# Kernel optimization log

Measured on AMD Instinct MI355X. Metric: run time of the kernel, lower is better.

## Reference

```python
import jax, jax.numpy as jnp
import numpy as np
from jax import lax

H, P, N, G, K, CHUNK = 64, 64, 128, 1, 4, 256
D_MODEL = 2048
D_INNER = H * P            # 4096
CONV_DIM = D_INNER + 2 * G * N  # 4352
EPS = 1e-5


def setup_inputs() -> dict:
    key = jax.random.key(0)
    ks = jax.random.split(key, 6)
    s = lambda k, shape, scale: jax.random.normal(k, shape, jnp.float32) * scale
    return {
        "hidden_states": s(ks[0], (2, 2048, D_MODEL), 1.0),
        "in_proj_w": s(ks[1], (D_MODEL, D_INNER + CONV_DIM + H), D_MODEL ** -0.5),
        "conv_w": s(ks[2], (CONV_DIM, K), K ** -0.5),
        "conv_b": jnp.zeros((CONV_DIM,), jnp.float32),
        "dt_bias": jnp.ones((H,), jnp.float32),
        "A_log": jnp.log(jnp.arange(1, H + 1, dtype=jnp.float32)),
        "D_param": jnp.ones((H,), jnp.float32),
        "norm_w": jnp.ones((D_INNER,), jnp.float32),
        "out_proj_w": s(ks[3], (D_INNER, D_MODEL), D_INNER ** -0.5),
    }


def _mamba2_forward(hidden_states, in_proj_w, conv_w, conv_b, dt_bias, A_log, D_param, norm_w, out_proj_w):
    b, l, _ = hidden_states.shape
    c = l // CHUNK  # number of chunks

    # in_proj -> gate | conv channels (x,B,C) | dt
    proj = hidden_states @ in_proj_w
    gate = proj[..., :D_INNER]
    hbc = proj[..., D_INNER:D_INNER + CONV_DIM]
    dt = proj[..., D_INNER + CONV_DIM:]  # [b,l,H]

    # depthwise causal conv1d + silu
    xt = hbc.transpose(0, 2, 1)  # [b, CONV_DIM, l]
    y = lax.conv_general_dilated(
        xt, conv_w[:, None, :], window_strides=(1,), padding=[(K - 1, 0)],
        feature_group_count=CONV_DIM, dimension_numbers=("NCH", "OIH", "NCH"))
    hbc = jax.nn.silu(y + conv_b[None, :, None]).transpose(0, 2, 1)  # [b,l,CONV_DIM]

    # split into x / B / C per group (unflatten over groups as in torch code)
    per_g = D_INNER // G
    hg = hbc.reshape(b, l, G, per_g + 2 * N)
    x = hg[..., :per_g].reshape(b, l, H, P)                 # [b,l,h,p]
    Bm = hg[..., per_g:per_g + N]                            # [b,l,g,n]
    Cm = hg[..., per_g + N:]                                 # [b,l,g,n]
    hpg = H // G
    Bh = jnp.repeat(Bm, hpg, axis=2)                         # [b,l,h,n]
    Ch = jnp.repeat(Cm, hpg, axis=2)

    # dt: softplus(dt + bias), clamp per time_step_limit (0, inf)
    dt = jax.nn.softplus(dt + dt_bias)                       # [b,l,h]
    A = -jnp.exp(A_log)                                      # [h]

    # chunk the sequence
    x_c = x.reshape(b, c, CHUNK, H, P)
    B_c = Bh.reshape(b, c, CHUNK, H, N)
    C_c = Ch.reshape(b, c, CHUNK, H, N)
    dt_c = dt.reshape(b, c, CHUNK, H)

    dA = dt_c * A[None, None, None, :]                       # [b,c,L,h]
    cum = jnp.cumsum(dA, axis=2)                             # [b,c,L,h]

    # intra-chunk (diagonal block): decay[i,j] = exp(cum_i - cum_j), i>=j
    diff = cum[:, :, :, None, :] - cum[:, :, None, :, :]     # [b,c,i,j,h]
    i = jnp.arange(CHUNK)
    mask = i[:, None] >= i[None, :]
    decay = jnp.exp(jnp.where(mask[None, None, :, :, None], diff, -jnp.inf))
    scores = jnp.einsum("bcihn,bcjhn->bcijh", C_c, B_c) * decay * dt_c[:, :, None, :, :]
    Y_diag = jnp.einsum("bcijh,bcjhp->bcihp", scores, x_c)   # [b,c,L,h,p]

    # per-chunk final states
    decay_states = jnp.exp(cum[:, :, -1:, :] - cum)          # [b,c,L,h]
    states = jnp.einsum("bclh,bclhn,bclhp->bchpn", decay_states * dt_c, B_c, x_c)
    chunk_decay = jnp.exp(cum[:, :, -1, :])                  # [b,c,h]

    # inter-chunk recurrence over chunks
    def step(prev, inp):
        st, cd = inp  # [b,h,p,n], [b,h]
        new = cd[:, :, None, None] * prev + st
        return new, prev

    init = jnp.zeros((b, H, P, N), hidden_states.dtype)
    _, prev_states = lax.scan(step, init, (jnp.moveaxis(states, 1, 0), jnp.moveaxis(chunk_decay, 1, 0)))
    prev_states = jnp.moveaxis(prev_states, 0, 1)            # [b,c,h,p,n]

    state_decay_out = jnp.exp(cum)                           # [b,c,L,h]
    Y_off = jnp.einsum("bclhn,bchpn,bclh->bclhp", C_c, prev_states, state_decay_out)

    yh = (Y_diag + Y_off).reshape(b, l, H, P) + D_param[None, None, :, None] * x
    yr = yh.reshape(b, l, D_INNER)

    # gated RMSNorm
    hidden = yr * jax.nn.silu(gate)
    var = jnp.mean(hidden * hidden, axis=-1, keepdims=True)
    hidden = hidden * lax.rsqrt(var + EPS) * norm_w

    return hidden @ out_proj_w


def reference(hidden_states, in_proj_w, conv_w, conv_b, dt_bias, A_log, D_param, norm_w, out_proj_w):
    return _mamba2_forward(hidden_states, in_proj_w, conv_w, conv_b, dt_bias, A_log, D_param, norm_w, out_proj_w)
```

## Files before the change

### kernel.cpp

```cpp
#include <hip/hip_runtime.h>
#include <hip/hip_bf16.h>


typedef __attribute__((ext_vector_type(8))) _Float16 f16x8;
typedef __attribute__((ext_vector_type(4))) float f32x4;

#define GLD16(gp, lp) __builtin_amdgcn_global_load_lds( \
    (__attribute__((address_space(1))) void*)(gp),      \
    (__attribute__((address_space(3))) void*)(lp), 16, 0, 0)

__device__ __forceinline__ unsigned short f2h(float v) {
  _Float16 h = (_Float16)v;
  return *reinterpret_cast<unsigned short*>(&h);
}
__device__ __forceinline__ float h2f(unsigned short u) {
  _Float16 h = *reinterpret_cast<_Float16*>(&u);
  return (float)h;
}
__device__ __forceinline__ float siluf(float x) { return x / (1.f + expf(-x)); }

__global__ __launch_bounds__(256) void cast_f16(const float* __restrict__ s,
                                                _Float16* __restrict__ d) {
  long i = ((long)blockIdx.x * 256 + threadIdx.x) * 4;
  float4 v = *reinterpret_cast<const float4*>(s + i);
  ushort4 u;
  u.x = f2h(v.x); u.y = f2h(v.y); u.z = f2h(v.z); u.w = f2h(v.w);
  *reinterpret_cast<ushort4*>(d + i) = u;
}

__global__ __launch_bounds__(256) void transpose_win(const float* __restrict__ src,
                                                     _Float16* __restrict__ dst) {
  __shared__ float tile[32][33];
  int c0 = blockIdx.x * 32, r0 = blockIdx.y * 32;
  int tx = threadIdx.x, ty = threadIdx.y;
#pragma unroll
  for (int i = 0; i < 4; i++)
    tile[ty + i * 8][tx] = src[(long)(r0 + ty + i * 8) * 8512 + c0 + tx];
  __syncthreads();
#pragma unroll
  for (int i = 0; i < 4; i++) {
    int c = c0 + ty + i * 8, r = r0 + tx;
    dst[(long)c * 2048 + r] = (_Float16)tile[tx][ty + i * 8];
  }
}

__global__ __launch_bounds__(256) void transpose_wout(const float* __restrict__ src,
                                                      _Float16* __restrict__ dst,
                                                      int R, int C) {
  __shared__ float tile[32][33];
  int c0 = blockIdx.x * 32, r0 = blockIdx.y * 32;
  int tx = threadIdx.x, ty = threadIdx.y;
#pragma unroll
  for (int i = 0; i < 4; i++)
    tile[ty + i * 8][tx] = src[(long)(r0 + ty + i * 8) * C + c0 + tx];
  __syncthreads();
#pragma unroll
  for (int i = 0; i < 4; i++) {
    int c = c0 + ty + i * 8, r = r0 + tx;
    dst[(long)c * R + r] = (_Float16)tile[tx][ty + i * 8];
  }
}

__global__ __launch_bounds__(512, 2) void gemm_in8(const _Float16* __restrict__ A,
                                                   const _Float16* __restrict__ Bt,
                                                   _Float16* __restrict__ gate,
                                                   float* __restrict__ hbcf) {
  __shared__ char ldsB[131072];
  const int tid = threadIdx.x;
  const int lane = tid & 63;
  const int wv = tid >> 6;
  const int wr = wv >> 2, wc = wv & 3;
  const int wg = blockIdx.x;
  const int swz = (wg & 7) * 66 + (wg >> 3);
  const int bx = swz % 33, by = swz / 33;

  const int srow = tid >> 3;
  const int scolg = (tid & 7) ^ ((srow & 4) >> 1);
  const _Float16* Ab = A + (long)by * 256 * 2048 + (long)srow * 2048 + scolg * 8;
  const _Float16* Bb = Bt + (long)bx * 256 * 2048 + (long)srow * 2048 + scolg * 8;
  const int ldst = tid << 4;

#define STAGE_A(tau, h) do {                                              \
    const _Float16* g_ = Ab + (long)(h) * 262144 + (tau) * 64;            \
    char* l_ = ldsB + ((((tau) & 1) << 2) + (h)) * 16384 + ldst;          \
    GLD16(g_, l_); GLD16(g_ + 131072, l_ + 8192); } while (0)
#define STAGE_B(tau, h) do {                                              \
    const _Float16* g_ = Bb + (long)(h) * 262144 + (tau) * 64;            \
    char* l_ = ldsB + ((((tau) & 1) << 2) + 2 + (h)) * 16384 + ldst;      \
    GLD16(g_, l_); GLD16(g_ + 131072, l_ + 8192); } while (0)

  const int fr = lane & 15;
  const int fkA = (lane >> 4) ^ ((fr & 4) ? 2 : 0);
  const char* aRd = ldsB + wr * 16384 + fr * 128 + fkA * 16;
  const char* bRd = ldsB + (2 + (wc >> 1)) * 16384 + ((wc & 1) * 64 + fr) * 128 + fkA * 16;
#define RD_A(b, mi, k32) (*(const f16x8*)(aRd + (b) * 65536 + (mi) * 2048 + (k32) * 64))
#define RD_B(b, ni, k32) (*(const f16x8*)(bRd + (b) * 65536 + (ni) * 2048 + (k32) * 64))

#define BAR() __builtin_amdgcn_s_barrier()
#define WLG0() asm volatile("s_waitcnt lgkmcnt(0)" ::: "memory")
#define WLG8() asm volatile("s_waitcnt lgkmcnt(8)" ::: "memory")
#define WVM4() asm volatile("s_waitcnt vmcnt(4)" ::: "memory")

  f32x4 acc[8][4];
#pragma unroll
  for (int mi = 0; mi < 8; ++mi)
#pragma unroll
    for (int ni = 0; ni < 4; ++ni) acc[mi][ni] = f32x4{0.f, 0.f, 0.f, 0.f};

  STAGE_A(0, 0); STAGE_A(0, 1); STAGE_B(0, 0); STAGE_B(0, 1);
  STAGE_B(1, 0); STAGE_B(1, 1);
  WVM4(); BAR();

#define MFMA_Q(MI0, MI1, x0, x1, x2, x3, PB)                                        \
  __builtin_amdgcn_s_setprio(1);                                                    \
  _Pragma("unroll") for (int ni = 0; ni < 4; ++ni) {                                \
    acc[MI0][ni] = __builtin_amdgcn_mfma_f32_16x16x32_f16(x0, PB[ni][0], acc[MI0][ni], 0, 0, 0); \
    acc[MI0][ni] = __builtin_amdgcn_mfma_f32_16x16x32_f16(x1, PB[ni][1], acc[MI0][ni], 0, 0, 0); \
    acc[MI1][ni] = __builtin_amdgcn_mfma_f32_16x16x32_f16(x2, PB[ni][0], acc[MI1][ni], 0, 0, 0); \
    acc[MI1][ni] = __builtin_amdgcn_mfma_f32_16x16x32_f16(x3, PB[ni][1], acc[MI1][ni], 0, 0, 0); \
  }                                                                                 \
  __builtin_amdgcn_s_setprio(0);

  for (int u = 0; u < 16; ++u) {
    const int t1 = 2 * u + 1;
    const int t2 = (2 * u + 2) & 31;
    const int t3 = (2 * u + 3) & 31;
    f16x8 PB0[4][2];
#pragma unroll
    for (int ni = 0; ni < 4; ++ni) { PB0[ni][0] = RD_B(0, ni, 0); PB0[ni][1] = RD_B(0, ni, 1); }
    {
      f16x8 x0 = RD_A(0, 0, 0), x1 = RD_A(0, 0, 1), x2 = RD_A(0, 1, 0), x3 = RD_A(0, 1, 1);
      STAGE_A(t1, 0); WLG8(); BAR(); WLG0();
      MFMA_Q(0, 1, x0, x1, x2, x3, PB0) BAR();
    }
    {
      f16x8 x0 = RD_A(0, 2, 0), x1 = RD_A(0, 2, 1), x2 = RD_A(0, 3, 0), x3 = RD_A(0, 3, 1);
      STAGE_A(t1, 1); BAR(); WLG0();
      MFMA_Q(2, 3, x0, x1, x2, x3, PB0) BAR();
    }
    {
      f16x8 x0 = RD_A(0, 4, 0), x1 = RD_A(0, 4, 1), x2 = RD_A(0, 5, 0), x3 = RD_A(0, 5, 1);
      STAGE_B(t2, 0); BAR(); WLG0();
      MFMA_Q(4, 5, x0, x1, x2, x3, PB0) BAR();
    }
    {
      f16x8 x0 = RD_A(0, 6, 0), x1 = RD_A(0, 6, 1), x2 = RD_A(0, 7, 0), x3 = RD_A(0, 7, 1);
      STAGE_B(t2, 1); BAR(); WLG0();
      MFMA_Q(6, 7, x0, x1, x2, x3, PB0) WVM4(); BAR();
    }
    f16x8 PB1[4][2];
#pragma unroll
    for (int ni = 0; ni < 4; ++ni) { PB1[ni][0] = RD_B(1, ni, 0); PB1[ni][1] = RD_B(1, ni, 1); }
    {
      f16x8 x0 = RD_A(1, 0, 0), x1 = RD_A(1, 0, 1), x2 = RD_A(1, 1, 0), x3 = RD_A(1, 1, 1);
      STAGE_A(t2, 0); WLG8(); BAR(); WLG0();
      MFMA_Q(0, 1, x0, x1, x2, x3, PB1) BAR();
    }
    {
      f16x8 x0 = RD_A(1, 2, 0), x1 = RD_A(1, 2, 1), x2 = RD_A(1, 3, 0), x3 = RD_A(1, 3, 1);
      STAGE_A(t2, 1); BAR(); WLG0();
      MFMA_Q(2, 3, x0, x1, x2, x3, PB1) BAR();
    }
    {
      f16x8 x0 = RD_A(1, 4, 0), x1 = RD_A(1, 4, 1), x2 = RD_A(1, 5, 0), x3 = RD_A(1, 5, 1);
      STAGE_B(t3, 0); BAR(); WLG0();
      MFMA_Q(4, 5, x0, x1, x2, x3, PB1) BAR();
    }
    {
      f16x8 x0 = RD_A(1, 6, 0), x1 = RD_A(1, 6, 1), x2 = RD_A(1, 7, 0), x3 = RD_A(1, 7, 1);
      STAGE_B(t3, 1); BAR(); WLG0();
      MFMA_Q(6, 7, x0, x1, x2, x3, PB1) WVM4(); BAR();
    }
  }
  const int m0 = by * 256 + wr * 128;
  const int n0 = bx * 256 + wc * 64;
  const int cl = lane & 15, rq = (lane >> 4) * 4;
  if (bx < 16) {
#pragma unroll
    for (int mi = 0; mi < 8; ++mi)
#pragma unroll
      for (int r = 0; r < 4; ++r) {
        long rowoff = (long)(m0 + mi * 16 + rq + r) * 4096 + n0 + cl;
#pragma unroll
        for (int ni = 0; ni < 4; ++ni) gate[rowoff + ni * 16] = (_Float16)acc[mi][ni][r];
      }
  } else {
#pragma unroll
    for (int mi = 0; mi < 8; ++mi)
#pragma unroll
      for (int r = 0; r < 4; ++r) {
        long rowoff = (long)(m0 + mi * 16 + rq + r) * 4352 + (n0 - 4096) + cl;
#pragma unroll
        for (int ni = 0; ni < 4; ++ni) hbcf[rowoff + ni * 16] = acc[mi][ni][r];
      }
  }
#undef STAGE_A
#undef STAGE_B
#undef RD_A
#undef RD_B
#undef BAR
#undef WLG0
#undef WLG8
#undef WVM4
#undef MFMA_Q
}

__global__ __launch_bounds__(256) void gemm_bt(const _Float16* __restrict__ A,
                                               const _Float16* __restrict__ Bt,
                                               float* __restrict__ Cf,
                                               int K, int ldc,
                                               long zsA, long zsB, long zsC) {
  __shared__ uint4 As4[512];
  __shared__ uint4 Bs4[512];
  _Float16* As = (_Float16*)As4;
  _Float16* Bs = (_Float16*)Bs4;
  const int tid = threadIdx.x;
  const int wv = tid >> 6;
  const int lane = tid & 63;
  const _Float16* Ab = A + (long)blockIdx.z * zsA + (long)blockIdx.y * 128 * K;
  const _Float16* Bb = Bt + (long)blockIdx.z * zsB + (long)blockIdx.x * 128 * K;
  const int c0 = wv * 128 + lane;
  const int c1 = c0 + 64;
  const long ra0 = (long)(c0 >> 2) * K + (c0 & 3) * 8;
  const long ra1 = (long)(c1 >> 2) * K + (c1 & 3) * 8;
  f32x4 acc[4][4];
#pragma unroll
  for (int mi = 0; mi < 4; mi++)
#pragma unroll
    for (int ni = 0; ni < 4; ni++) acc[mi][ni] = f32x4{0.f, 0.f, 0.f, 0.f};
  const int mrow = (wv & 1) * 64 + (lane & 15);
  const int nrow = (wv >> 1) * 64 + (lane & 15);
  const int koff = (lane >> 4) * 8;
  for (int k0 = 0; k0 < K; k0 += 32) {
    GLD16(Ab + ra0 + k0, (char*)As + c0 * 16);
    GLD16(Ab + ra1 + k0, (char*)As + c1 * 16);
    GLD16(Bb + ra0 + k0, (char*)Bs + c0 * 16);
    GLD16(Bb + ra1 + k0, (char*)Bs + c1 * 16);
    __syncthreads();
    f16x8 af[4], bfr[4];
#pragma unroll
    for (int mi = 0; mi < 4; mi++)
      af[mi] = *(const f16x8*)(As + (mrow + mi * 16) * 32 + koff);
#pragma unroll
    for (int ni = 0; ni < 4; ni++)
      bfr[ni] = *(const f16x8*)(Bs + (nrow + ni * 16) * 32 + koff);
#pragma unroll
    for (int mi = 0; mi < 4; mi++)
#pragma unroll
      for (int ni = 0; ni < 4; ni++)
        acc[mi][ni] = __builtin_amdgcn_mfma_f32_16x16x32_f16(af[mi], bfr[ni],
                                                             acc[mi][ni], 0, 0, 0);
    __syncthreads();
  }
  const int m0 = blockIdx.y * 128 + (wv & 1) * 64;
  const int n0 = blockIdx.x * 128 + (wv >> 1) * 64;
  const int cl = lane & 15, rq = (lane >> 4) * 4;
  const long zc = (long)blockIdx.z * zsC;
#pragma unroll
  for (int mi = 0; mi < 4; mi++)
#pragma unroll
    for (int r = 0; r < 4; r++) {
      long rowoff = zc + (long)(m0 + mi * 16 + rq + r) * ldc + n0 + cl;
#pragma unroll
      for (int ni = 0; ni < 4; ni++) Cf[rowoff + ni * 16] = acc[mi][ni][r];
    }
}

__global__ __launch_bounds__(256) void dtz_kernel(const float* __restrict__ hs,
                                                  const float* __restrict__ Win,
                                                  float* __restrict__ zf) {
  __shared__ float Xs[4][2048];
  int t0 = blockIdx.x * 4;
  int tid = threadIdx.x;
#pragma unroll
  for (int i = 0; i < 8; i++) {
    int e = tid * 4 + i * 1024;
    int tok = e >> 11, k = e & 2047;
    *reinterpret_cast<float4*>(&Xs[tok][k]) =
        *reinterpret_cast<const float4*>(&hs[(long)(t0 + tok) * 2048 + k]);
  }
  __syncthreads();
  int h = tid & 63, tg = tid >> 6;
  float a0 = 0.f, a1 = 0.f, a2 = 0.f, a3 = 0.f;
  const float* wcol = Win + 8448 + h;
  for (int k = 0; k < 2048; k += 4) {
    a0 = fmaf(Xs[tg][k + 0], wcol[(long)(k + 0) * 8512], a0);
    a1 = fmaf(Xs[tg][k + 1], wcol[(long)(k + 1) * 8512], a1);
    a2 = fmaf(Xs[tg][k + 2], wcol[(long)(k + 2) * 8512], a2);
    a3 = fmaf(Xs[tg][k + 3], wcol[(long)(k + 3) * 8512], a3);
  }
  zf[(long)(t0 + tg) * 64 + h] = (a0 + a1) + (a2 + a3);
}

__global__ __launch_bounds__(256) void conv_silu_kernel(const float* __restrict__ hbcf,
                                                        const float* __restrict__ convw,
                                                        const float* __restrict__ convb,
                                                        _Float16* __restrict__ x16,
                                                        _Float16* __restrict__ B16,
                                                        _Float16* __restrict__ C16) {
  int q = blockIdx.x * 256 + threadIdx.x;
  int t = blockIdx.y;
  int l = t & 2047;
  const float* col = hbcf + (long)t * 4352 + q;
  float4 wq = *reinterpret_cast<const float4*>(convw + q * 4);
  float a = convb[q];
  if (l >= 3) a += col[-3 * 4352] * wq.x;
  if (l >= 2) a += col[-2 * 4352] * wq.y;
  if (l >= 1) a += col[-1 * 4352] * wq.z;
  a += col[0] * wq.w;
  _Float16 o = (_Float16)siluf(a);
  if (q < 4096) x16[(long)t * 4096 + q] = o;
  else if (q < 4224) B16[(long)t * 128 + (q - 4096)] = o;
  else C16[(long)t * 128 + (q - 4224)] = o;
}

__global__ __launch_bounds__(256) void xtrans(const unsigned short* __restrict__ src,
                                              unsigned short* __restrict__ dst) {
  __shared__ unsigned short tile[64][66];
  int c0 = blockIdx.x * 64, r0 = blockIdx.y * 64;
  int tx = threadIdx.x & 15, ty = threadIdx.x >> 4;
#pragma unroll
  for (int i = 0; i < 4; i++) {
    int r = ty + i * 16;
    ushort4 v = *(const ushort4*)&src[(long)(r0 + r) * 4096 + c0 + 4 * tx];
    tile[r][4 * tx] = v.x; tile[r][4 * tx + 1] = v.y;
    tile[r][4 * tx + 2] = v.z; tile[r][4 * tx + 3] = v.w;
  }
  __syncthreads();
#pragma unroll
  for (int i = 0; i < 4; i++) {
    int c = ty + i * 16;
    ushort4 v;
    v.x = tile[4 * tx + 0][c]; v.y = tile[4 * tx + 1][c];
    v.z = tile[4 * tx + 2][c]; v.w = tile[4 * tx + 3][c];
    *(ushort4*)&dst[(long)(c0 + c) * 4096 + r0 + 4 * tx] = v;
  }
}

__global__ __launch_bounds__(256) void dt_cum_kernel(const float* __restrict__ zf,
                                                     const float* __restrict__ dtb,
                                                     const float* __restrict__ Alog,
                                                     float* __restrict__ dt_f,
                                                     float* __restrict__ cum_f,
                                                     float* __restrict__ cuml) {
  int bc = blockIdx.x;
  int h = threadIdx.x & 63, seg = threadIdx.x >> 6;
  int t0 = bc * 256;
  float Ah = -expf(Alog[h]);
  float bias = dtb[h];
  __shared__ float segsum[4][64];
  float s = 0.f;
  for (int j = 0; j < 64; j++) {
    int t = t0 + seg * 64 + j;
    float z = zf[(long)t * 64 + h] + bias;
    float v = (z > 20.f) ? z : log1pf(expf(z));
    dt_f[(long)t * 64 + h] = v;
    s += v * Ah;
  }
  segsum[seg][h] = s;
  __syncthreads();
  float run = 0.f;
  for (int k = 0; k < seg; k++) run += segsum[k][h];
  for (int j = 0; j < 64; j++) {
    int t = t0 + seg * 64 + j;
    run += dt_f[(long)t * 64 + h] * Ah;
    cum_f[(long)t * 64 + h] = run;
  }
  if (seg == 3) cuml[bc * 64 + h] = run;
}

__global__ __launch_bounds__(256) void states_mfma(const unsigned short* __restrict__ xT16,
                                                   const unsigned short* __restrict__ B16,
                                                   const float* __restrict__ dt_f,
                                                   const float* __restrict__ cum_f,
                                                   const float* __restrict__ cuml,
                                                   float* __restrict__ states) {
  int h = blockIdx.x, bc = blockIdx.y;
  int t0 = bc * 256, tid = threadIdx.x;
  __shared__ float w_s[256];
  __shared__ unsigned short Aw[64 * 40];
  __shared__ unsigned short BT[128 * 40];
  {
    int t = t0 + tid;
    w_s[tid] = expf(cuml[bc * 64 + h] - cum_f[(long)t * 64 + h]) * dt_f[(long)t * 64 + h];
  }
  __syncthreads();
  int wv = tid >> 6, lane = tid & 63;
  int mr = lane & 15, koff = (lane >> 4) * 8;
  f32x4 acc[4][2];
#pragma unroll
  for (int mi = 0; mi < 4; mi++)
#pragma unroll
    for (int nj = 0; nj < 2; nj++) acc[mi][nj] = f32x4{0.f, 0.f, 0.f, 0.f};
  for (int kt = 0; kt < 8; kt++) {
    {
      int p = tid >> 2, tq = tid & 3;
      const unsigned short* g = &xT16[((long)(h * 64 + p)) * 4096 + t0 + kt * 32 + tq * 8];
      ushort4 u0 = *(const ushort4*)g, u1 = *(const ushort4*)(g + 4);
      const float* wp = &w_s[kt * 32 + tq * 8];
      ushort4 o0, o1;
      o0.x = f2h(h2f(u0.x) * wp[0]); o0.y = f2h(h2f(u0.y) * wp[1]);
      o0.z = f2h(h2f(u0.z) * wp[2]); o0.w = f2h(h2f(u0.w) * wp[3]);
      o1.x = f2h(h2f(u1.x) * wp[4]); o1.y = f2h(h2f(u1.y) * wp[5]);
      o1.z = f2h(h2f(u1.z) * wp[6]); o1.w = f2h(h2f(u1.w) * wp[7]);
      *(ushort4*)&Aw[p * 40 + tq * 8] = o0;
      *(ushort4*)&Aw[p * 40 + tq * 8 + 4] = o1;
    }
    {
      int tl = tid >> 3, ng = tid & 7;
      const unsigned short* g = &B16[((long)(t0 + kt * 32 + tl)) * 128 + ng * 16];
#pragma unroll
      for (int j = 0; j < 16; j++) BT[(ng * 16 + j) * 40 + tl] = g[j];
    }
    __syncthreads();
    f16x8 af[4], bf[2];
#pragma unroll
    for (int mi = 0; mi < 4; mi++)
      af[mi] = *(const f16x8*)&Aw[(mi * 16 + mr) * 40 + koff];
#pragma unroll
    for (int nj = 0; nj < 2; nj++)
      bf[nj] = *(const f16x8*)&BT[((wv * 2 + nj) * 16 + mr) * 40 + koff];
#pragma unroll
    for (int mi = 0; mi < 4; mi++)
#pragma unroll
      for (int nj = 0; nj < 2; nj++)
        acc[mi][nj] = __builtin_amdgcn_mfma_f32_16x16x32_f16(af[mi], bf[nj],
                                                             acc[mi][nj], 0, 0, 0);
    __syncthreads();
  }
  int cl = lane & 15, rq = (lane >> 4) * 4;
  long base = ((long)(bc * 64 + h)) * 8192;
#pragma unroll
  for (int mi = 0; mi < 4; mi++)
#pragma unroll
    for (int r = 0; r < 4; r++) {
      int p = mi * 16 + rq + r;
#pragma unroll
      for (int nj = 0; nj < 2; nj++) {
        int n = (wv * 2 + nj) * 16 + cl;
        states[base + p * 128 + n] = acc[mi][nj][r];
      }
    }
}

__global__ __launch_bounds__(256) void recur_kernel(float* __restrict__ states,
                                                    const float* __restrict__ cuml) {
  int bh = blockIdx.x;
  int b = bh >> 6, h = bh & 63;
  int tid = threadIdx.x;
  float4 prev[8];
#pragma unroll
  for (int j = 0; j < 8; j++) prev[j] = make_float4(0.f, 0.f, 0.f, 0.f);
  for (int c = 0; c < 8; c++) {
    int bc = b * 8 + c;
    float cd = expf(cuml[bc * 64 + h]);
    long base = (long)(bc * 64 + h) * 8192;
#pragma unroll
    for (int j = 0; j < 8; j++) {
      long o = base + j * 1024 + tid * 4;
      float4 st = *reinterpret_cast<const float4*>(&states[o]);
      *reinterpret_cast<float4*>(&states[o]) = prev[j];
      prev[j].x = fmaf(cd, prev[j].x, st.x);
      prev[j].y = fmaf(cd, prev[j].y, st.y);
      prev[j].z = fmaf(cd, prev[j].z, st.z);
      prev[j].w = fmaf(cd, prev[j].w, st.w);
    }
  }
}

__global__ __launch_bounds__(256) void yfused(const unsigned short* __restrict__ xT16,
                                              const unsigned short* __restrict__ x16,
                                              const unsigned short* __restrict__ C16,
                                              const float* __restrict__ CBT,
                                              const float* __restrict__ states,
                                              const float* __restrict__ dt_f,
                                              const float* __restrict__ cum_f,
                                              const float* __restrict__ Dp,
                                              float* __restrict__ Ysum) {
  int h = blockIdx.x, bc = blockIdx.y;
  int t0 = bc * 256, tid = threadIdx.x;
  __shared__ unsigned short Sb[256 * 40];
  __shared__ unsigned short Xb[64 * 264];
  __shared__ float cum_s[256], dt_s[256];
  int i = tid;
  cum_s[i] = cum_f[(long)(t0 + i) * 64 + h];
  dt_s[i] = dt_f[(long)(t0 + i) * 64 + h];
  {
    int p = tid >> 2, tq = tid & 3;
    const unsigned short* g = &xT16[((long)(h * 64 + p)) * 4096 + t0 + tq * 64];
    unsigned short* l = &Xb[p * 264 + tq * 64];
#pragma unroll
    for (int c = 0; c < 8; c++)
      *(uint4*)(l + c * 8) = *(const uint4*)(g + c * 8);
  }
  __syncthreads();
  float cum_i = cum_s[i];
  const float* cbrow = CBT + (long)bc * 65536 + (long)i * 256;
  int wv = tid >> 6, lane = tid & 63;
  int mr = lane & 15, koff = (lane >> 4) * 8;
  f32x4 acc[4][4];
#pragma unroll
  for (int mi = 0; mi < 4; mi++)
#pragma unroll
    for (int ni = 0; ni < 4; ni++) acc[mi][ni] = f32x4{0.f, 0.f, 0.f, 0.f};
  for (int kt = 0; kt < 8; kt++) {
    int k0 = kt * 32;
#pragma unroll
    for (int c = 0; c < 8; c++) {
      float4 cb = *(const float4*)&cbrow[k0 + c * 4];
      ushort4 o;
      {
        int j = k0 + c * 4 + 0;
        float s = (j <= i) ? cb.x * expf(cum_i - cum_s[j]) * dt_s[j] : 0.f;
        o.x = f2h(s);
      }
      {
        int j = k0 + c * 4 + 1;
        float s = (j <= i) ? cb.y * expf(cum_i - cum_s[j]) * dt_s[j] : 0.f;
        o.y = f2h(s);
      }
      {
        int j = k0 + c * 4 + 2;
        float s = (j <= i) ? cb.z * expf(cum_i - cum_s[j]) * dt_s[j] : 0.f;
        o.z = f2h(s);
      }
      {
        int j = k0 + c * 4 + 3;
        float s = (j <= i) ? cb.w * expf(cum_i - cum_s[j]) * dt_s[j] : 0.f;
        o.w = f2h(s);
      }
      *(ushort4*)&Sb[i * 40 + c * 4] = o;
    }
    __syncthreads();
    if (kt <= 2 * wv + 1) {
      f16x8 af[4], bf[4];
#pragma unroll
      for (int mi = 0; mi < 4; mi++)
        af[mi] = *(const f16x8*)&Sb[(64 * wv + mi * 16 + mr) * 40 + koff];
#pragma unroll
      for (int ni = 0; ni < 4; ni++)
        bf[ni] = *(const f16x8*)&Xb[(ni * 16 + mr) * 264 + k0 + koff];
#pragma unroll
      for (int mi = 0; mi < 4; mi++)
#pragma unroll
        for (int ni = 0; ni < 4; ni++)
          acc[mi][ni] = __builtin_amdgcn_mfma_f32_16x16x32_f16(af[mi], bf[ni],
                                                               acc[mi][ni], 0, 0, 0);
    }
    __syncthreads();
  }
  {
    int p = tid >> 2, nq = tid & 3;
    const float* g = &states[((long)(bc * 64 + h)) * 8192 + p * 128 + nq * 32];
    unsigned short* l = &Xb[p * 136 + nq * 32];
#pragma unroll
    for (int c = 0; c < 8; c++) {
      float4 v = *(const float4*)(g + c * 4);
      ushort4 u;
      u.x = f2h(v.x); u.y = f2h(v.y); u.z = f2h(v.z); u.w = f2h(v.w);
      *(ushort4*)(l + c * 4) = u;
    }
  }
  float fac_i = expf(cum_i);
  for (int kn = 0; kn < 4; kn++) {
    {
      const unsigned short* g = &C16[((long)(t0 + i)) * 128 + kn * 32];
#pragma unroll
      for (int c = 0; c < 8; c++) {
        ushort4 u = *(const ushort4*)(g + c * 4);
        ushort4 o;
        o.x = f2h(h2f(u.x) * fac_i); o.y = f2h(h2f(u.y) * fac_i);
        o.z = f2h(h2f(u.z) * fac_i); o.w = f2h(h2f(u.w) * fac_i);
        *(ushort4*)&Sb[i * 40 + c * 4] = o;
      }
    }
    __syncthreads();
    f16x8 af[4], bf[4];
#pragma unroll
    for (int mi = 0; mi < 4; mi++)
      af[mi] = *(const f16x8*)&Sb[(64 * wv + mi * 16 + mr) * 40 + koff];
#pragma unroll
    for (int ni = 0; ni < 4; ni++)
      bf[ni] = *(const f16x8*)&Xb[(ni * 16 + mr) * 136 + kn * 32 + koff];
#pragma unroll
    for (int mi = 0; mi < 4; mi++)
#pragma unroll
      for (int ni = 0; ni < 4; ni++)
        acc[mi][ni] = __builtin_amdgcn_mfma_f32_16x16x32_f16(af[mi], bf[ni],
                                                             acc[mi][ni], 0, 0, 0);
    __syncthreads();
  }
  float Dh = Dp[h];
  int cl = lane & 15, rq = (lane >> 4) * 4;
#pragma unroll
  for (int mi = 0; mi < 4; mi++)
#pragma unroll
    for (int r = 0; r < 4; r++) {
      long row = t0 + 64 * wv + mi * 16 + rq + r;
      float* yr = &Ysum[row * 4096 + h * 64];
      const unsigned short* xr = &x16[row * 4096 + h * 64];
#pragma unroll
      for (int ni = 0; ni < 4; ni++) {
        int p = ni * 16 + cl;
        yr[p] = acc[mi][ni][r] + Dh * h2f(xr[p]);
      }
    }
}

__global__ __launch_bounds__(256) void norm_kernel(const float* __restrict__ Ysum,
                                                   const _Float16* __restrict__ gate,
                                                   const float* __restrict__ nw,
                                                   _Float16* __restrict__ hid) {
  int t = blockIdx.x;
  int tid = threadIdx.x;
  float hv[16];
  float ss = 0.f;
#pragma unroll
  for (int k = 0; k < 4; k++) {
    int d = tid * 4 + k * 1024;
    float4 y = *reinterpret_cast<const float4*>(&Ysum[(long)t * 4096 + d]);
    ushort4 gu = *reinterpret_cast<const ushort4*>(gate + (long)t * 4096 + d);
    float h0 = y.x * siluf(h2f(gu.x)), h1 = y.y * siluf(h2f(gu.y));
    float h2 = y.z * siluf(h2f(gu.z)), h3 = y.w * siluf(h2f(gu.w));
    hv[k * 4 + 0] = h0; hv[k * 4 + 1] = h1; hv[k * 4 + 2] = h2; hv[k * 4 + 3] = h3;
    ss += h0 * h0 + h1 * h1 + h2 * h2 + h3 * h3;
  }
#pragma unroll
  for (int o = 32; o > 0; o >>= 1) ss += __shfl_down(ss, o, 64);
  __shared__ float ws4[4];
  if ((tid & 63) == 0) ws4[tid >> 6] = ss;
  __syncthreads();
  float var = (ws4[0] + ws4[1] + ws4[2] + ws4[3]) * (1.f / 4096.f);
  float scale = rsqrtf(var + 1e-5f);
#pragma unroll
  for (int k = 0; k < 4; k++) {
    int d = tid * 4 + k * 1024;
    ushort4 u;
#pragma unroll
    for (int c = 0; c < 4; c++)
      ((unsigned short*)&u)[c] = f2h(hv[k * 4 + c] * scale * nw[d + c]);
    *reinterpret_cast<ushort4*>(hid + (long)t * 4096 + d) = u;
  }
}

extern "C" void kernel_launch(void* const* d_in, const int* in_sizes, int n_in,
                              void* d_out, int out_size, void* d_ws, size_t ws_size,
                              hipStream_t stream) {
  (void)in_sizes; (void)n_in; (void)out_size; (void)ws_size;
  const float* hs    = (const float*)d_in[0];
  const float* Win   = (const float*)d_in[1];
  const float* convw = (const float*)d_in[2];
  const float* convb = (const float*)d_in[3];
  const float* dtb   = (const float*)d_in[4];
  const float* Alog  = (const float*)d_in[5];
  const float* Dp    = (const float*)d_in[6];
  const float* nw    = (const float*)d_in[7];
  const float* Wout  = (const float*)d_in[8];
  float* out = (float*)d_out;

  char* base = (char*)d_ws;
  size_t off = 0;
  auto take = [&](size_t n) { char* r = base + off; off += (n + 255) & ~(size_t)255; return r; };
  float*    hbcf  = (float*)take(4096UL * 4352 * 4);
  _Float16* gateh = (_Float16*)take(4096UL * 4096 * 2);
  _Float16* Ah    = (_Float16*)take(4096UL * 2048 * 2);
  _Float16* WtH   = (_Float16*)take(8448UL * 2048 * 2);
  _Float16* xT16  = (_Float16*)take(4096UL * 4096 * 2);
  _Float16* B16   = (_Float16*)take(4096UL * 128 * 2);
  _Float16* C16   = (_Float16*)take(4096UL * 128 * 2);
  float*    zf    = (float*)take(4096UL * 64 * 4);
  float*    dt_f  = (float*)take(4096UL * 64 * 4);
  float*    cum_f = (float*)take(4096UL * 64 * 4);
  float*    cuml  = (float*)take(16UL * 64 * 4);
  float*    CBT   = (float*)take(16UL * 256 * 256 * 4);
  float*    states= (float*)take(1024UL * 8192 * 4);
  float*    Ysum  = hbcf;
  _Float16* WoutT = Ah;
  _Float16* x16   = WtH;
  _Float16* hid   = (_Float16*)states;

  dim3 tb(32, 8);
  cast_f16<<<8192, 256, 0, stream>>>(hs, Ah);
  transpose_win<<<dim3(264, 64), tb, 0, stream>>>(Win, WtH);
  dtz_kernel<<<1024, 256, 0, stream>>>(hs, Win, zf);
  gemm_in8<<<dim3(528), 512, 0, stream>>>(Ah, WtH, gateh, hbcf);
  transpose_wout<<<dim3(64, 128), tb, 0, stream>>>(Wout, WoutT, 4096, 2048);
  conv_silu_kernel<<<dim3(17, 4096), 256, 0, stream>>>(hbcf, convw, convb, x16, B16, C16);
  dt_cum_kernel<<<16, 256, 0, stream>>>(zf, dtb, Alog, dt_f, cum_f, cuml);
  xtrans<<<dim3(64, 64), 256, 0, stream>>>((const unsigned short*)x16, (unsigned short*)xT16);
  gemm_bt<<<dim3(2, 2, 16), 256, 0, stream>>>(C16, B16, CBT, 128, 256,
                                              32768, 32768, 65536);
  states_mfma<<<dim3(64, 16), 256, 0, stream>>>((const unsigned short*)xT16,
                                                (const unsigned short*)B16,
                                                dt_f, cum_f, cuml, states);
  recur_kernel<<<128, 256, 0, stream>>>(states, cuml);
  yfused<<<dim3(64, 16), 256, 0, stream>>>((const unsigned short*)xT16,
                                           (const unsigned short*)x16,
                                           (const unsigned short*)C16,
                                           CBT, states, dt_f, cum_f, Dp, Ysum);
  norm_kernel<<<4096, 256, 0, stream>>>(Ysum, gateh, nw, hid);
  gemm_bt<<<dim3(16, 32, 1), 256, 0, stream>>>(hid, WoutT, out, 4096, 2048, 0, 0, 0);
}
```

Baseline: 832.5 us.

## Use pipelined 256x256 MFMA GEMM with split-K for out_proj and full XOR swizzle

Replaces the generic 128x128 gemm_bt for the output projection with a dedicated 8-wave 256x256-tile kernel that stages tiles via direct-to-LDS loads. It splits K=4096 into two halves written to separate fp32 partial buffers, then sums them in a small add kernel. The LDS swizzle in both the in-proj and out-proj GEMMs changes from a partial 2-bit XOR to a full 3-bit XOR on row index, which should cut LDS bank conflicts. The cost is an extra 2x32MB partial write and read plus an additional kernel launch.

```diff
diff --git a/kernel.cpp b/kernel.cpp
--- a/kernel.cpp
+++ b/kernel.cpp
@@ -65,7 +65,7 @@
                                                    const _Float16* __restrict__ Bt,
                                                    _Float16* __restrict__ gate,
                                                    float* __restrict__ hbcf) {
-  __shared__ char ldsB[131072];
+  __shared__ __attribute__((aligned(128))) char ldsB[131072];
   const int tid = threadIdx.x;
   const int lane = tid & 63;
   const int wv = tid >> 6;
@@ -75,7 +75,7 @@
   const int bx = swz % 33, by = swz / 33;
 
   const int srow = tid >> 3;
-  const int scolg = (tid & 7) ^ ((srow & 4) >> 1);
+  const int scolg = (tid & 7) ^ (srow & 7);
   const _Float16* Ab = A + (long)by * 256 * 2048 + (long)srow * 2048 + scolg * 8;
   const _Float16* Bb = Bt + (long)bx * 256 * 2048 + (long)srow * 2048 + scolg * 8;
   const int ldst = tid << 4;
@@ -90,11 +90,11 @@
     GLD16(g_, l_); GLD16(g_ + 131072, l_ + 8192); } while (0)
 
   const int fr = lane & 15;
-  const int fkA = (lane >> 4) ^ ((fr & 4) ? 2 : 0);
-  const char* aRd = ldsB + wr * 16384 + fr * 128 + fkA * 16;
-  const char* bRd = ldsB + (2 + (wc >> 1)) * 16384 + ((wc & 1) * 64 + fr) * 128 + fkA * 16;
-#define RD_A(b, mi, k32) (*(const f16x8*)(aRd + (b) * 65536 + (mi) * 2048 + (k32) * 64))
-#define RD_B(b, ni, k32) (*(const f16x8*)(bRd + (b) * 65536 + (ni) * 2048 + (k32) * 64))
+  const int c16 = (lane >> 4) ^ (fr & 7);
+  const int aOff = wr * 16384 + fr * 128 + c16 * 16;
+  const int bOff = (2 + (wc >> 1)) * 16384 + ((wc & 1) * 64 + fr) * 128 + c16 * 16;
+#define RD_A(b, mi, k32) (*(const f16x8*)(ldsB + ((aOff + (b) * 65536 + (mi) * 2048) ^ ((k32) * 64))))
+#define RD_B(b, ni, k32) (*(const f16x8*)(ldsB + ((bOff + (b) * 65536 + (ni) * 2048) ^ ((k32) * 64))))
 
 #define BAR() __builtin_amdgcn_s_barrier()
 #define WLG0() asm volatile("s_waitcnt lgkmcnt(0)" ::: "memory")
@@ -198,11 +198,138 @@
 #undef STAGE_B
 #undef RD_A
 #undef RD_B
+}
+
+__global__ __launch_bounds__(512, 2) void gemm_out8(const _Float16* __restrict__ A,
+                                                    const _Float16* __restrict__ Bt,
+                                                    float* __restrict__ Cp) {
+  __shared__ __attribute__((aligned(128))) char ldsB[131072];
+  const int tid = threadIdx.x;
+  const int lane = tid & 63;
+  const int wv = tid >> 6;
+  const int wr = wv >> 2, wc = wv & 3;
+  const int wg = blockIdx.x;
+  const int z = wg >> 7;
+  const int r7 = wg & 127;
+  const int sw = (r7 & 7) * 16 + (r7 >> 3);
+  const int by = sw >> 3, bx = sw & 7;
+
+  const int srow = tid >> 3;
+  const int scolg = (tid & 7) ^ (srow & 7);
+  const _Float16* Ab = A + (long)by * 256 * 4096 + (long)z * 2048 +
+                       (long)srow * 4096 + scolg * 8;
+  const _Float16* Bb = Bt + (long)bx * 256 * 4096 + (long)z * 2048 +
+                       (long)srow * 4096 + scolg * 8;
+  const int ldst = tid << 4;
+
+#define STAGE_A(tau, h) do {                                              \
+    const _Float16* g_ = Ab + (long)(h) * 524288 + (tau) * 64;            \
+    char* l_ = ldsB + ((((tau) & 1) << 2) + (h)) * 16384 + ldst;          \
+    GLD16(g_, l_); GLD16(g_ + 262144, l_ + 8192); } while (0)
+#define STAGE_B(tau, h) do {                                              \
+    const _Float16* g_ = Bb + (long)(h) * 524288 + (tau) * 64;            \
+    char* l_ = ldsB + ((((tau) & 1) << 2) + 2 + (h)) * 16384 + ldst;      \
+    GLD16(g_, l_); GLD16(g_ + 262144, l_ + 8192); } while (0)
+
+  const int fr = lane & 15;
+  const int c16 = (lane >> 4) ^ (fr & 7);
+  const int aOff = wr * 16384 + fr * 128 + c16 * 16;
+  const int bOff = (2 + (wc >> 1)) * 16384 + ((wc & 1) * 64 + fr) * 128 + c16 * 16;
+#define RD_A(b, mi, k32) (*(const f16x8*)(ldsB + ((aOff + (b) * 65536 + (mi) * 2048) ^ ((k32) * 64))))
+#define RD_B(b, ni, k32) (*(const f16x8*)(ldsB + ((bOff + (b) * 65536 + (ni) * 2048) ^ ((k32) * 64))))
+
+  f32x4 acc[8][4];
+#pragma unroll
+  for (int mi = 0; mi < 8; ++mi)
+#pragma unroll
+    for (int ni = 0; ni < 4; ++ni) acc[mi][ni] = f32x4{0.f, 0.f, 0.f, 0.f};
+
+  STAGE_A(0, 0); STAGE_A(0, 1); STAGE_B(0, 0); STAGE_B(0, 1);
+  STAGE_B(1, 0); STAGE_B(1, 1);
+  WVM4(); BAR();
+
+  for (int u = 0; u < 16; ++u) {
+    const int t1 = 2 * u + 1;
+    const int t2 = (2 * u + 2) & 31;
+    const int t3 = (2 * u + 3) & 31;
+    f16x8 PB0[4][2];
+#pragma unroll
+    for (int ni = 0; ni < 4; ++ni) { PB0[ni][0] = RD_B(0, ni, 0); PB0[ni][1] = RD_B(0, ni, 1); }
+    {
+      f16x8 x0 = RD_A(0, 0, 0), x1 = RD_A(0, 0, 1), x2 = RD_A(0, 1, 0), x3 = RD_A(0, 1, 1);
+      STAGE_A(t1, 0); WLG8(); BAR(); WLG0();
+      MFMA_Q(0, 1, x0, x1, x2, x3, PB0) BAR();
+    }
+    {
+      f16x8 x0 = RD_A(0, 2, 0), x1 = RD_A(0, 2, 1), x2 = RD_A(0, 3, 0), x3 = RD_A(0, 3, 1);
+      STAGE_A(t1, 1); BAR(); WLG0();
+      MFMA_Q(2, 3, x0, x1, x2, x3, PB0) BAR();
+    }
+    {
+      f16x8 x0 = RD_A(0, 4, 0), x1 = RD_A(0, 4, 1), x2 = RD_A(0, 5, 0), x3 = RD_A(0, 5, 1);
+      STAGE_B(t2, 0); BAR(); WLG0();
+      MFMA_Q(4, 5, x0, x1, x2, x3, PB0) BAR();
+    }
+    {
+      f16x8 x0 = RD_A(0, 6, 0), x1 = RD_A(0, 6, 1), x2 = RD_A(0, 7, 0), x3 = RD_A(0, 7, 1);
+      STAGE_B(t2, 1); BAR(); WLG0();
+      MFMA_Q(6, 7, x0, x1, x2, x3, PB0) WVM4(); BAR();
+    }
+    f16x8 PB1[4][2];
+#pragma unroll
+    for (int ni = 0; ni < 4; ++ni) { PB1[ni][0] = RD_B(1, ni, 0); PB1[ni][1] = RD_B(1, ni, 1); }
+    {
+      f16x8 x0 = RD_A(1, 0, 0), x1 = RD_A(1, 0, 1), x2 = RD_A(1, 1, 0), x3 = RD_A(1, 1, 1);
+      STAGE_A(t2, 0); WLG8(); BAR(); WLG0();
+      MFMA_Q(0, 1, x0, x1, x2, x3, PB1) BAR();
+    }
+    {
+      f16x8 x0 = RD_A(1, 2, 0), x1 = RD_A(1, 2, 1), x2 = RD_A(1, 3, 0), x3 = RD_A(1, 3, 1);
+      STAGE_A(t2, 1); BAR(); WLG0();
+      MFMA_Q(2, 3, x0, x1, x2, x3, PB1) BAR();
+    }
+    {
+      f16x8 x0 = RD_A(1, 4, 0), x1 = RD_A(1, 4, 1), x2 = RD_A(1, 5, 0), x3 = RD_A(1, 5, 1);
+      STAGE_B(t3, 0); BAR(); WLG0();
+      MFMA_Q(4, 5, x0, x1, x2, x3, PB1) BAR();
+    }
+    {
+      f16x8 x0 = RD_A(1, 6, 0), x1 = RD_A(1, 6, 1), x2 = RD_A(1, 7, 0), x3 = RD_A(1, 7, 1);
+      STAGE_B(t3, 1); BAR(); WLG0();
+      MFMA_Q(6, 7, x0, x1, x2, x3, PB1) WVM4(); BAR();
+    }
+  }
+  const int m0 = by * 256 + wr * 128;
+  const int n0 = bx * 256 + wc * 64;
+  const int cl = lane & 15, rq = (lane >> 4) * 4;
+  float* Cb = Cp + (long)z * 8388608;
+#pragma unroll
+  for (int mi = 0; mi < 8; ++mi)
+#pragma unroll
+    for (int r = 0; r < 4; ++r) {
+      long rowoff = (long)(m0 + mi * 16 + rq + r) * 2048 + n0 + cl;
+#pragma unroll
+      for (int ni = 0; ni < 4; ++ni) Cb[rowoff + ni * 16] = acc[mi][ni][r];
+    }
+#undef STAGE_A
+#undef STAGE_B
+#undef RD_A
+#undef RD_B
 #undef BAR
 #undef WLG0
 #undef WLG8
 #undef WVM4
 #undef MFMA_Q
+}
+
+__global__ __launch_bounds__(256) void add_out(const float* __restrict__ p,
+                                               float* __restrict__ o) {
+  long i = ((long)blockIdx.x * 256 + threadIdx.x) * 4;
+  float4 a = *reinterpret_cast<const float4*>(p + i);
+  float4 b = *reinterpret_cast<const float4*>(p + 8388608 + i);
+  float4 r;
+  r.x = a.x + b.x; r.y = a.y + b.y; r.z = a.z + b.z; r.w = a.w + b.w;
+  *reinterpret_cast<float4*>(o + i) = r;
 }
 
 __global__ __launch_bounds__(256) void gemm_bt(const _Float16* __restrict__ A,
@@ -675,6 +802,7 @@
   float*    CBT   = (float*)take(16UL * 256 * 256 * 4);
   float*    states= (float*)take(1024UL * 8192 * 4);
   float*    Ysum  = hbcf;
+  float*    oparts= hbcf;
   _Float16* WoutT = Ah;
   _Float16* x16   = WtH;
   _Float16* hid   = (_Float16*)states;
@@ -699,5 +827,6 @@
                                            (const unsigned short*)C16,
                                            CBT, states, dt_f, cum_f, Dp, Ysum);
   norm_kernel<<<4096, 256, 0, stream>>>(Ysum, gateh, nw, hid);
-  gemm_bt<<<dim3(16, 32, 1), 256, 0, stream>>>(hid, WoutT, out, 4096, 2048, 0, 0, 0);
-}
+  gemm_out8<<<dim3(256), 512, 0, stream>>>(hid, WoutT, oparts);
+  add_out<<<8192, 256, 0, stream>>>(oparts, out);
+}
```

Result: faster. 787.2 us (-5.4%).
